# Performance work log

Hardware: AMD Instinct MI355X
Metric: run time of the kernel (lower is better)

Reference implementation:

```python
import jax, jax.numpy as jnp
import numpy as np

H, W = 200, 200            # image_size
X_RANGE = (0.0, 100.0)
Y_RANGE = (0.0, 100.0)
SIZE = 36                   # kernel 'size' from source
SIGMA = 3.0
K = SIZE + 1                # kernel is 37x37 (arange(-18, 19))


def _gaussian_kernel():
    r = jnp.arange(-(SIZE // 2), SIZE // 2 + 1, dtype=jnp.float32)
    k1 = jnp.exp(-(r ** 2) / (2.0 * SIGMA ** 2))
    k2 = k1[:, None] * k1[None, :]
    return k2 / k2.sum()    # [K, K]


def setup_inputs() -> dict:
    key = jax.random.key(0)
    # trajectory coords in world units [0, 100) -> spread over whole map
    x_t = jax.random.uniform(key, (512, 64, 2), dtype=jnp.float32) * 100.0
    return {"x_t": x_t}


def reference(x_t):
    B, T, _ = x_t.shape
    x_scale = W / (X_RANGE[1] - X_RANGE[0])
    y_scale = H / (Y_RANGE[1] - Y_RANGE[0])
    # .long() in torch truncates toward zero; inputs are >= 0 here so astype(int32) matches
    x_pix = ((x_t[:, :, 0] - X_RANGE[0]) * x_scale).astype(jnp.int32)   # [B, T]
    y_pix = H - ((x_t[:, :, 1] - Y_RANGE[0]) * y_scale).astype(jnp.int32)
    valid = ~(jnp.isnan(x_t[:, :, 0]) | jnp.isnan(x_t[:, :, 1]))        # [B, T]

    half = SIZE // 2
    x_start = jnp.clip(x_pix - half, 0, W - SIZE)
    y_start = jnp.clip(y_pix - half, 0, H - SIZE)
    x_end = jnp.clip(x_pix + half, 0, W)
    y_end = jnp.clip(y_pix + half, 0, H)
    kx = x_end - x_start    # patch width  (<= 36, kernel[:,:kx] = top-left slice)
    ky = y_end - y_start    # patch height

    kern = _gaussian_kernel()                       # [K, K]
    r = jnp.arange(K)
    c = jnp.arange(K)
    # mask: kernel[:ky, :kx] slice, and point validity            [B, T, K, K]
    mask = ((r[None, None, :, None] < ky[..., None, None])
            & (c[None, None, None, :] < kx[..., None, None])
            & valid[..., None, None])
    vals = jnp.where(mask, kern[None, None, :, :], 0.0)            # [B, T, K, K]
    rows = jnp.clip(y_start[..., None, None] + r[None, None, :, None], 0, H - 1)
    cols = jnp.clip(x_start[..., None, None] + c[None, None, None, :], 0, W - 1)
    rows = jnp.broadcast_to(rows, (B, T, K, K))
    cols = jnp.broadcast_to(cols, (B, T, K, K))
    flat = (rows * W + cols).reshape(B, -1)                        # [B, T*K*K]

    # parallel scatter-add splat of all Gaussian patches
    heat = jnp.zeros((B, H * W), jnp.float32)
    heat = heat.at[jnp.arange(B)[:, None], flat].add(vals.reshape(B, -1))
    heat = heat.reshape(B, H, W)

    # per-image max normalization (max over dim1 then dim2 == max over both)
    m = heat.max(axis=(1, 2), keepdims=True)
    return heat / (m + 1e-10)
```

## Files before the change

### kernel.cpp

```cpp
#include <hip/hip_runtime.h>


#define NT 64
#define TDIM 224
#define NTL 7
#define BLK 448

typedef short bf16x8 __attribute__((ext_vector_type(8)));
typedef float f32x16 __attribute__((ext_vector_type(16)));

static __device__ inline unsigned f2bf(float f) {
    unsigned int u = __float_as_uint(f);
    u = (u + 0x7FFFu + ((u >> 16) & 1u)) >> 16;
    return u & 0xFFFFu;
}

struct __align__(16) SMem {
    unsigned short Rm[TDIM][64];
    unsigned short Cm[TDIM][64];
    float wmax[NTL];
};

__global__ __launch_bounds__(BLK) void heatmap_kernel(const float* __restrict__ x_t,
                                                      float* __restrict__ out) {
    __shared__ SMem s;
    const int tid  = threadIdx.x;
    const int lane = tid & 63;
    const int wv   = tid >> 6;
    const int b    = blockIdx.x;

    float ssum = 0.0f;
    #pragma unroll
    for (int i = 0; i < 37; ++i) {
        float r = (float)(i - 18);
        ssum += expf(-(r * r) * (1.0f / 18.0f));
    }
    const float invs = 1.0f / ssum;

    {
        const int q4 = tid & 15;
        const int rg = tid >> 4;
        const float4 p01 = *(const float4*)(x_t + (size_t)b * 128 + 8 * q4);
        const float4 p23 = *(const float4*)(x_t + (size_t)b * 128 + 8 * q4 + 4);
        float px[4] = {p01.x, p01.z, p23.x, p23.z};
        float py[4] = {p01.y, p01.w, p23.y, p23.w};
        int xs[4], ys[4], kx[4], ky[4];
        #pragma unroll
        for (int k = 0; k < 4; ++k) {
            bool valid = (px[k] == px[k]) && (py[k] == py[k]);
            int xp = (int)(px[k] * 2.0f);
            int yp = 200 - (int)(py[k] * 2.0f);
            xs[k] = min(max(xp - 18, 0), 164);
            ys[k] = min(max(yp - 18, 0), 164);
            kx[k] = valid ? (min(max(xp + 18, 0), 200) - xs[k]) : 0;
            ky[k] = valid ? (min(max(yp + 18, 0), 200) - ys[k]) : 0;
        }
        #pragma unroll
        for (int i = 0; i < 8; ++i) {
            const int row = rg + 28 * i;
            const int off = (8 * q4) ^ ((row & 7) << 4);
            unsigned rv[4], cv[4];
            #pragma unroll
            for (int k = 0; k < 4; ++k) {
                int d = row - ys[k];
                float fd = (float)(d - 18);
                float v = expf(-(fd * fd) * (1.0f / 18.0f)) * invs;
                rv[k] = ((unsigned)d < (unsigned)ky[k]) ? f2bf(v) : 0u;
                int e = row - xs[k];
                float fe = (float)(e - 18);
                float w = expf(-(fe * fe) * (1.0f / 18.0f)) * invs;
                cv[k] = ((unsigned)e < (unsigned)kx[k]) ? f2bf(w) : 0u;
            }
            uint2 R = {rv[0] | (rv[1] << 16), rv[2] | (rv[3] << 16)};
            *(uint2*)((char*)s.Rm + row * 128 + off) = R;
            uint2 C = {cv[0] | (cv[1] << 16), cv[2] | (cv[3] << 16)};
            *(uint2*)((char*)s.Cm + row * 128 + off) = C;
        }
    }
    __syncthreads();

    const int swl = (lane & 7) << 4;

    bf16x8 Bf[4];
    {
        const char* rb = (const char*)s.Rm + (wv * 32 + (lane & 31)) * 128;
        #pragma unroll
        for (int m = 0; m < 4; ++m)
            Bf[m] = *(const bf16x8*)(rb + ((16 * (2 * m + (lane >> 5))) ^ swl));
    }

    float gmax = 0.0f;
    for (int tx = 0; tx < NTL; ++tx) {
        const char* ab = (const char*)s.Cm + (tx * 32 + (lane & 31)) * 128;
        f32x16 acc;
        #pragma unroll
        for (int r = 0; r < 16; ++r) acc[r] = 0.0f;
        #pragma unroll
        for (int m = 0; m < 4; ++m) {
            bf16x8 Af = *(const bf16x8*)(ab + ((16 * (2 * m + (lane >> 5))) ^ swl));
            acc = __builtin_amdgcn_mfma_f32_32x32x16_bf16(Af, Bf[m], acc, 0, 0, 0);
        }
        #pragma unroll
        for (int r = 0; r < 16; ++r) gmax = fmaxf(gmax, acc[r]);
    }
    #pragma unroll
    for (int off = 32; off > 0; off >>= 1) gmax = fmaxf(gmax, __shfl_xor(gmax, off));
    if (lane == 0) s.wmax[wv] = gmax;
    __syncthreads();
    float mm = s.wmax[0];
    #pragma unroll
    for (int w = 1; w < NTL; ++w) mm = fmaxf(mm, s.wmax[w]);
    const float scale = 1.0f / (mm + 1e-10f);

    float* ob = out + (size_t)b * (200 * 200);
    const int y  = wv * 32 + (lane & 31);
    const int xh = 4 * (lane >> 5);
    for (int tx = 0; tx < NTL; ++tx) {
        const char* ab = (const char*)s.Cm + (tx * 32 + (lane & 31)) * 128;
        f32x16 acc;
        #pragma unroll
        for (int r = 0; r < 16; ++r) acc[r] = 0.0f;
        #pragma unroll
        for (int m = 0; m < 4; ++m) {
            bf16x8 Af = *(const bf16x8*)(ab + ((16 * (2 * m + (lane >> 5))) ^ swl));
            acc = __builtin_amdgcn_mfma_f32_32x32x16_bf16(Af, Bf[m], acc, 0, 0, 0);
        }
        if (y < 200) {
            #pragma unroll
            for (int g = 0; g < 4; ++g) {
                const int x0 = tx * 32 + 8 * g + xh;
                if (x0 < 200) {
                    float4 v = {acc[4 * g] * scale, acc[4 * g + 1] * scale,
                                acc[4 * g + 2] * scale, acc[4 * g + 3] * scale};
                    *(float4*)(ob + (size_t)y * 200 + x0) = v;
                }
            }
        }
    }
}

extern "C" void kernel_launch(void* const* d_in, const int* in_sizes, int n_in,
                              void* d_out, int out_size, void* d_ws, size_t ws_size,
                              hipStream_t stream) {
    const float* x_t = (const float*)d_in[0];
    float* out = (float*)d_out;
    const int B = in_sizes[0] / (NT * 2);
    heatmap_kernel<<<B, BLK, 0, stream>>>(x_t, out);
}
```

Baseline: 27.58 us.

## Stage output tiles through shared memory for row-contiguous coalesced stores

The output pass swaps operand roles so each wave owns a 32-column strip and loops over row tiles. Results are staged into a shared-memory strip of 16 full rows, and the block then writes contiguous float4 rows to global memory. This replaces the earlier scattered float4 stores, which touched 7 different row segments per wave, with fully coalesced row writes. The cost is extra shared memory, two block-wide barriers per half-tile, and an LDS round trip.

After: 28.39 us. 2.9% more time.

```diff
diff --git a/kernel.cpp b/kernel.cpp
--- a/kernel.cpp
+++ b/kernel.cpp
@@ -18,6 +18,7 @@
 struct __align__(16) SMem {
     unsigned short Rm[TDIM][64];
     unsigned short Cm[TDIM][64];
+    float strip[16][TDIM];
     float wmax[NTL];
 };
 
@@ -81,27 +82,26 @@
 
     const int swl = (lane & 7) << 4;
 
-    bf16x8 Bf[4];
+    float gmax = 0.0f;
     {
-        const char* rb = (const char*)s.Rm + (wv * 32 + (lane & 31)) * 128;
+        bf16x8 Af[4];
+        const char* ab = (const char*)s.Rm + (wv * 32 + (lane & 31)) * 128;
         #pragma unroll
         for (int m = 0; m < 4; ++m)
-            Bf[m] = *(const bf16x8*)(rb + ((16 * (2 * m + (lane >> 5))) ^ swl));
-    }
-
-    float gmax = 0.0f;
-    for (int tx = 0; tx < NTL; ++tx) {
-        const char* ab = (const char*)s.Cm + (tx * 32 + (lane & 31)) * 128;
-        f32x16 acc;
-        #pragma unroll
-        for (int r = 0; r < 16; ++r) acc[r] = 0.0f;
-        #pragma unroll
-        for (int m = 0; m < 4; ++m) {
-            bf16x8 Af = *(const bf16x8*)(ab + ((16 * (2 * m + (lane >> 5))) ^ swl));
-            acc = __builtin_amdgcn_mfma_f32_32x32x16_bf16(Af, Bf[m], acc, 0, 0, 0);
+            Af[m] = *(const bf16x8*)(ab + ((16 * (2 * m + (lane >> 5))) ^ swl));
+        for (int tx = 0; tx < NTL; ++tx) {
+            const char* bb = (const char*)s.Cm + (tx * 32 + (lane & 31)) * 128;
+            f32x16 acc;
+            #pragma unroll
+            for (int r = 0; r < 16; ++r) acc[r] = 0.0f;
+            #pragma unroll
+            for (int m = 0; m < 4; ++m) {
+                bf16x8 Bf = *(const bf16x8*)(bb + ((16 * (2 * m + (lane >> 5))) ^ swl));
+                acc = __builtin_amdgcn_mfma_f32_32x32x16_bf16(Af[m], Bf, acc, 0, 0, 0);
+            }
+            #pragma unroll
+            for (int r = 0; r < 16; ++r) gmax = fmaxf(gmax, acc[r]);
         }
-        #pragma unroll
-        for (int r = 0; r < 16; ++r) gmax = fmaxf(gmax, acc[r]);
     }
     #pragma unroll
     for (int off = 32; off > 0; off >>= 1) gmax = fmaxf(gmax, __shfl_xor(gmax, off));
@@ -112,28 +112,42 @@
     for (int w = 1; w < NTL; ++w) mm = fmaxf(mm, s.wmax[w]);
     const float scale = 1.0f / (mm + 1e-10f);
 
+    bf16x8 Bf2[4];
+    {
+        const char* cb = (const char*)s.Cm + (wv * 32 + (lane & 31)) * 128;
+        #pragma unroll
+        for (int m = 0; m < 4; ++m)
+            Bf2[m] = *(const bf16x8*)(cb + ((16 * (2 * m + (lane >> 5))) ^ swl));
+    }
     float* ob = out + (size_t)b * (200 * 200);
-    const int y  = wv * 32 + (lane & 31);
-    const int xh = 4 * (lane >> 5);
-    for (int tx = 0; tx < NTL; ++tx) {
-        const char* ab = (const char*)s.Cm + (tx * 32 + (lane & 31)) * 128;
+    for (int ty = 0; ty < NTL; ++ty) {
+        const char* ab = (const char*)s.Rm + (ty * 32 + (lane & 31)) * 128;
         f32x16 acc;
         #pragma unroll
         for (int r = 0; r < 16; ++r) acc[r] = 0.0f;
         #pragma unroll
         for (int m = 0; m < 4; ++m) {
             bf16x8 Af = *(const bf16x8*)(ab + ((16 * (2 * m + (lane >> 5))) ^ swl));
-            acc = __builtin_amdgcn_mfma_f32_32x32x16_bf16(Af, Bf[m], acc, 0, 0, 0);
+            acc = __builtin_amdgcn_mfma_f32_32x32x16_bf16(Af, Bf2[m], acc, 0, 0, 0);
         }
-        if (y < 200) {
+        #pragma unroll
+        for (int h = 0; h < 2; ++h) {
+            const int ybase = ty * 32 + 16 * h;
+            const int nrow  = min(16, 200 - ybase);
+            if (nrow <= 0) continue;
+            __syncthreads();
             #pragma unroll
-            for (int g = 0; g < 4; ++g) {
-                const int x0 = tx * 32 + 8 * g + xh;
-                if (x0 < 200) {
-                    float4 v = {acc[4 * g] * scale, acc[4 * g + 1] * scale,
-                                acc[4 * g + 2] * scale, acc[4 * g + 3] * scale};
-                    *(float4*)(ob + (size_t)y * 200 + x0) = v;
-                }
+            for (int rr = 0; rr < 8; ++rr) {
+                const int r  = rr + 8 * h;
+                const int yl = (r & 3) + 8 * ((r >> 2) & 1) + 4 * (lane >> 5);
+                s.strip[yl][32 * wv + (lane & 31)] = acc[r] * scale;
+            }
+            __syncthreads();
+            for (int id = tid; id < nrow * 50; id += BLK) {
+                const int yl = id / 50;
+                const int x4 = id - 50 * yl;
+                float4 v = *(const float4*)&s.strip[yl][4 * x4];
+                *(float4*)(ob + (size_t)(ybase + yl) * 200 + 4 * x4) = v;
             }
         }
     }
```
